# Kernel optimization log

Hardware: AMD Instinct MI355X
Metric: run time of the kernel (lower is better)

## Reference

```python
import jax, jax.numpy as jnp
import numpy as np

K = 5          # up_kernel
G = 1          # up_group
S = 2          # scale_factor


def conv2d(x, w, b, pad):
    y = jax.lax.conv_general_dilated(
        x, w, window_strides=(1, 1), padding=[(pad, pad), (pad, pad)],
        dimension_numbers=('NCHW', 'OIHW', 'NCHW'))
    return y + b[None, :, None, None]


def pixel_shuffle(x, r):
    n, c, h, w = x.shape
    x = x.reshape(n, c // (r * r), r, r, h, w)
    x = x.transpose(0, 1, 4, 2, 5, 3)  # n, c', h, r, w, r
    return x.reshape(n, c // (r * r), h * r, w * r)


def setup_inputs() -> dict:
    key = jax.random.key(0)
    k1, k2, k3 = jax.random.split(key, 3)
    x = jax.random.normal(k1, (8, 256, 64, 64), dtype=jnp.float32)
    w_comp = jax.random.normal(k2, (64, 256, 1, 1), dtype=jnp.float32) * 0.05
    b_comp = jnp.zeros((64,), dtype=jnp.float32)
    w_enc = jax.random.normal(k3, (100, 64, 3, 3), dtype=jnp.float32) * 0.001
    b_enc = jnp.zeros((100,), dtype=jnp.float32)
    return {"x": x, "w_comp": w_comp, "b_comp": b_comp, "w_enc": w_enc, "b_enc": b_enc}


def reference(x, w_comp, b_comp, w_enc, b_enc):
    n, c, h, w = x.shape
    kk = K * K
    # channel compressor (1x1) + content encoder (3x3, pad 1)
    comp = conv2d(x, w_comp, b_comp, pad=0)
    mask = conv2d(comp, w_enc, b_enc, pad=1)          # (n, kk*G*S*S, h, w)
    # kernel normalizer: pixel_shuffle then softmax over the kk taps
    mask = pixel_shuffle(mask, S)                      # (n, kk*G, H, W)
    H, W = h * S, w * S
    mask = mask.reshape(n, G, kk, H, W)
    mask = jax.nn.softmax(mask, axis=2)
    # CARAFE reassembly: each output pixel gathers KxK neighborhood of its
    # low-res source pixel (i//S, j//S) with the learned normalized weights.
    r = (K - 1) // 2
    xp = jnp.pad(x, ((0, 0), (0, 0), (r, r), (r, r)))
    cg = c // G
    out = jnp.zeros((n, c, H, W), dtype=x.dtype)
    for idx in range(kk):  # small fixed loop over kernel taps (25)
        dy, dx = idx // K, idx % K
        patch = xp[:, :, dy:dy + h, dx:dx + w]                     # (n,c,h,w)
        patch_up = jnp.repeat(jnp.repeat(patch, S, axis=2), S, axis=3)  # (n,c,H,W)
        wgt = mask[:, :, idx]                                      # (n,G,H,W)
        out = out + (patch_up.reshape(n, G, cg, H, W) * wgt[:, :, None]).reshape(n, c, H, W)
    return out
```

## Files before the change

kernel.cpp:

```cpp
#include <hip/hip_runtime.h>


#define CI 256

typedef __attribute__((ext_vector_type(8))) short bf16x8;
typedef __attribute__((ext_vector_type(4))) float f32x4;
typedef __attribute__((ext_vector_type(2))) float f32x2;

__device__ inline unsigned short f2bf(float f) {
    unsigned u = __float_as_uint(f);
    unsigned r = (u + 0x7FFF + ((u >> 16) & 1)) >> 16;
    return (unsigned short)r;
}

__device__ inline unsigned cvt_pk_bf16(float lo, float hi) {
    unsigned r;
    asm("v_cvt_pk_bf16_f32 %0, %1, %2" : "=v"(r) : "v"(lo), "v"(hi));
    return r;
}

__device__ inline float bf_lo(unsigned u) { return __int_as_float(u << 16); }
__device__ inline float bf_hi(unsigned u) { return __int_as_float(u & 0xffff0000u); }

__device__ inline void pk_fma_lo(f32x2& acc, f32x2 m, f32x2 s) {
    asm("v_pk_fma_f32 %0, %1, %2, %0 op_sel_hi:[1,0,1]" : "+v"(acc) : "v"(m), "v"(s));
}
__device__ inline void pk_fma_hi(f32x2& acc, f32x2 m, f32x2 s) {
    asm("v_pk_fma_f32 %0, %1, %2, %0 op_sel:[0,1,0] op_sel_hi:[1,1,1]" : "+v"(acc) : "v"(m), "v"(s));
}

__device__ inline void nt_store2(float* p, f32x2 v) {
    __builtin_nontemporal_store(__builtin_bit_cast(unsigned long long, v),
                                (unsigned long long*)p);
}

__global__ __launch_bounds__(256) void prep_small(const float* __restrict__ w_comp,
                                                  unsigned short* __restrict__ wA,
                                                  float* __restrict__ zp) {
    int i = blockIdx.x * 256 + threadIdx.x;
    if (i < 64) zp[i] = 0.f;
    if (i < 64 * 256) wA[i] = f2bf(w_comp[i]);
}

__global__ __launch_bounds__(64) void conv1x1_mfma(const float* __restrict__ x,
                                                   const unsigned short* __restrict__ wA,
                                                   const float* __restrict__ b_comp,
                                                   const float* __restrict__ w_enc,
                                                   unsigned short* __restrict__ comp,
                                                   unsigned short* __restrict__ Bp) {
    int l = threadIdx.x;
    int b = blockIdx.x;

    if (b >= 2048) {
        int idx = (b - 2048) * 64 + l;
        int j = idx & 7;
        int n = (idx >> 3) % 112;
        int g = idx / (112 * 8);
        int k = g * 8 + j;
        int tap = k >> 6;
        int c = k & 63;
        float v = (n < 100) ? w_enc[n * 576 + c * 9 + tap] : 0.f;
        Bp[idx] = f2bf(v);
        return;
    }

    int c16 = l & 15;
    int lq  = l >> 4;
    int bs  = (b & 7) * 256 + (b >> 3);
    int P0  = bs * 16;
    int nimg = P0 >> 12;
    int hw   = P0 & 4095;

    const float* xp = x + (size_t)nimg * CI * 4096 + hw + c16;

    f32x4 acc[4];
#pragma unroll
    for (int mt = 0; mt < 4; mt++) acc[mt] = f32x4{0.f, 0.f, 0.f, 0.f};

#pragma unroll
    for (int ks = 0; ks < 8; ks++) {
        int k0 = ks * 32 + lq * 8;
        float v[8];
#pragma unroll
        for (int j = 0; j < 8; j++) v[j] = xp[(size_t)(k0 + j) * 4096];
        bf16x8 xb;
#pragma unroll
        for (int j = 0; j < 8; j++) xb[j] = (short)f2bf(v[j]);
#pragma unroll
        for (int mt = 0; mt < 4; mt++) {
            bf16x8 wf = *(const bf16x8*)(wA + (mt * 16 + c16) * 256 + k0);
            acc[mt] = __builtin_amdgcn_mfma_f32_16x16x32_bf16(wf, xb, acc[mt], 0, 0, 0);
        }
    }

    unsigned short* cp = comp + (size_t)(P0 + c16) * 64;
#pragma unroll
    for (int mt = 0; mt < 4; mt++) {
        int och0 = mt * 16 + lq * 4;
        float4 bb = *reinterpret_cast<const float4*>(b_comp + och0);
        unsigned u0 = f2bf(acc[mt][0] + bb.x) | (f2bf(acc[mt][1] + bb.y) << 16);
        unsigned u1 = f2bf(acc[mt][2] + bb.z) | (f2bf(acc[mt][3] + bb.w) << 16);
        reinterpret_cast<uint2*>(cp + och0)[0] = uint2{u0, u1};
    }
}

__global__ __launch_bounds__(256) void conv3x3_mfma(const unsigned short* __restrict__ comp,
                                                    const unsigned short* __restrict__ Bp,
                                                    const float* __restrict__ b_enc,
                                                    const float* __restrict__ zp,
                                                    unsigned* __restrict__ maskP) {
    __shared__ char Bs[2][5 * 7168];
    int tid = threadIdx.x;
    int wv  = tid >> 6;
    int l   = tid & 63;
    int c16 = l & 15;
    int lq  = l >> 4;
    int b   = blockIdx.x;
    int bs  = (b & 7) * 64 + (b >> 3);
    int nimg = bs >> 6;
    int h    = bs & 63;
    int w0   = wv * 16;

    const char* cbase = (const char*)(comp + (size_t)nimg * 4096 * 64);
    const char* zpb   = (const char*)zp;
    const char* Bpb   = (const char*)Bp;

#define STAGEPH(s0_, cnt_, buf_)                                                          \
    {                                                                                     \
        const char* src_ = Bpb + (s0_)*7168 + l * 16;                                     \
        for (int inst_ = wv; inst_ < 7 * (cnt_); inst_ += 4) {                            \
            __builtin_amdgcn_global_load_lds(                                             \
                (const __attribute__((address_space(1))) void*)(src_ + inst_ * 1024),     \
                (__attribute__((address_space(3))) void*)(&Bs[buf_][inst_ * 1024]),       \
                16, 0, 0);                                                                \
        }                                                                                 \
    }

    f32x4 acc[7];
#pragma unroll
    for (int nt = 0; nt < 7; nt++) acc[nt] = f32x4{0.f, 0.f, 0.f, 0.f};

    const int dyt[9] = {-1, -1, -1, 0, 0, 0, 1, 1, 1};
    const int dxt[9] = {-1, 0, 1, -1, 0, 1, -1, 0, 1};

    STAGEPH(0, 5, 0);
    __syncthreads();

#pragma unroll
    for (int ph = 0; ph < 4; ph++) {
        int s0  = ph * 5;
        int cnt = (s0 + 5 <= 18) ? 5 : (18 - s0);
        int cur = ph & 1;
        if (ph < 3) {
            int ns0  = s0 + 5;
            int ncnt = (ns0 + 5 <= 18) ? 5 : (18 - ns0);
            STAGEPH(ns0, ncnt, cur ^ 1);
        }
        for (int ss = 0; ss < cnt; ss++) {
            int s = s0 + ss;
            int tap = s >> 1, half = s & 1;
            int hh = h + dyt[tap];
            int ww = w0 + c16 + dxt[tap];
            const char* ap = ((unsigned)hh < 64u && (unsigned)ww < 64u)
                                 ? cbase + (hh * 64 + ww) * 128 : zpb;
            bf16x8 a = *(const bf16x8*)(ap + lq * 16 + half * 64);

            bf16x8 bf[7];
#pragma unroll
            for (int nt = 0; nt < 7; nt++)
                bf[nt] = *(const bf16x8*)(&Bs[cur][ss * 7168 + (lq * 112 + nt * 16 + c16) * 16]);
#pragma unroll
            for (int nt = 0; nt < 7; nt++)
                acc[nt] = __builtin_amdgcn_mfma_f32_16x16x32_bf16(a, bf[nt], acc[nt], 0, 0, 0);
        }
        __syncthreads();
    }
#undef STAGEPH

    float bias[7];
#pragma unroll
    for (int nt = 0; nt < 7; nt++) {
        int n = nt * 16 + c16;
        bias[nt] = (n < 100) ? b_enc[n] : 0.f;
    }
    int nvalid = (c16 < 4) ? 7 : 6;

    unsigned* mbase = maskP + ((size_t)nimg * 64 + h) * 3200;

#pragma unroll
    for (int r = 0; r < 4; r++) {
        float v[7];
#pragma unroll
        for (int nt = 0; nt < 7; nt++) v[nt] = acc[nt][r] + bias[nt];
        float m = v[0];
#pragma unroll
        for (int nt = 1; nt < 7; nt++) if (nt < nvalid) m = fmaxf(m, v[nt]);
        m = fmaxf(m, __shfl_xor(m, 4));
        m = fmaxf(m, __shfl_xor(m, 8));
        float e[7];
        float s = 0.f;
#pragma unroll
        for (int nt = 0; nt < 7; nt++) {
            e[nt] = (nt < nvalid) ? __expf(v[nt] - m) : 0.f;
            s += e[nt];
        }
        s += __shfl_xor(s, 4);
        s += __shfl_xor(s, 8);
        float inv = 1.f / s;
        int wpix = w0 + lq * 4 + r;
#pragma unroll
        for (int nt = 0; nt < 7; nt++) {
            float mine = (nt < nvalid) ? e[nt] * inv : 0.f;
            float part = __shfl_xor(mine, 1);
            if (((c16 & 1) == 0) && (nt * 16 + c16) < 100) {
                unsigned pk = cvt_pk_bf16(mine, part);
                mbase[(nt * 8 + (c16 >> 1)) * 64 + wpix] = pk;
            }
        }
    }
}

__global__ __launch_bounds__(256) void reassemble(const float* __restrict__ x,
                                                  const unsigned* __restrict__ maskP,
                                                  float* __restrict__ out) {
    int lane = threadIdx.x & 63;
    int cq   = threadIdx.x >> 6;
    int b    = blockIdx.x;
    int bs   = (b & 7) * 256 + (b >> 3);
    int cgb  = bs & 3;
    int h    = (bs >> 2) & 63;
    int n    = bs >> 8;
    int c0   = cgb * 64 + cq * 16;

    const unsigned* mrow = maskP + ((size_t)n * 64 + h) * 3200 + lane;

    int   yy[5];
    float vmy[5], vmx[5];
#pragma unroll
    for (int d = 0; d < 5; d++) {
        int y  = h + d - 2;
        int xc = lane + d - 2;
        yy[d]  = min(max(y, 0), 63) * 64;
        vmy[d] = ((unsigned)y  < 64u) ? 1.f : 0.f;
        vmx[d] = ((unsigned)xc < 64u) ? 1.f : 0.f;
    }

    f32x2 msk2[50];
#pragma unroll
    for (int t = 0; t < 25; t++) {
        float f = vmy[t / 5] * vmx[t % 5];
        unsigned u0 = mrow[(2 * t + 0) * 64];
        unsigned u1 = mrow[(2 * t + 1) * 64];
        f32x2 m01, m23;
        m01.x = bf_lo(u0); m01.y = bf_hi(u0);
        m23.x = bf_lo(u1); m23.y = bf_hi(u1);
        msk2[2 * t + 0] = m01 * f;
        msk2[2 * t + 1] = m23 * f;
    }

    int idxm2 = ((lane - 2) & 63) << 2;
    int idxm1 = ((lane - 1) & 63) << 2;
    int idxp1 = ((lane + 1) & 63) << 2;
    int idxp2 = ((lane + 2) & 63) << 2;

    const float* xbase = x + ((size_t)(n * CI + c0)) * 4096 + lane;
    float*       obase = out + ((size_t)(n * CI + c0) * 128 + 2 * h) * 128 + 2 * lane;

    float ra[5], rb[5];
    unsigned pk[5];
#pragma unroll
    for (int d = 0; d < 5; d++) {
        ra[d] = xbase[yy[d]];
        rb[d] = xbase[4096 + yy[d]];
        pk[d] = cvt_pk_bf16(ra[d], rb[d]);
    }

    for (int p = 0; p < 8; p++) {
        const float* xn = xbase + (size_t)((p < 7) ? (2 * p + 2) : 0) * 4096;
        float na[5], nb[5];
#pragma unroll
        for (int d = 0; d < 5; d++) {
            na[d] = xn[yy[d]];
            nb[d] = xn[4096 + yy[d]];
        }

        f32x2 A0 = {0.f, 0.f}, A1 = {0.f, 0.f};
        f32x2 B0 = {0.f, 0.f}, B1 = {0.f, 0.f};
#pragma unroll
        for (int d = 0; d < 5; d++) {
            int pv = (int)pk[d];
            int sm2 = __builtin_amdgcn_ds_bpermute(idxm2, pv);
            int sm1 = __builtin_amdgcn_ds_bpermute(idxm1, pv);
            int sp1 = __builtin_amdgcn_ds_bpermute(idxp1, pv);
            int sp2 = __builtin_amdgcn_ds_bpermute(idxp2, pv);
            f32x2 s[5];
            s[0].x = bf_lo((unsigned)sm2); s[0].y = bf_hi((unsigned)sm2);
            s[1].x = bf_lo((unsigned)sm1); s[1].y = bf_hi((unsigned)sm1);
            s[2].x = ra[d];                s[2].y = rb[d];
            s[3].x = bf_lo((unsigned)sp1); s[3].y = bf_hi((unsigned)sp1);
            s[4].x = bf_lo((unsigned)sp2); s[4].y = bf_hi((unsigned)sp2);
            const f32x2* mk2 = msk2 + d * 10;
#pragma unroll
            for (int k = 0; k < 5; k++) {
                pk_fma_lo(A0, mk2[2 * k + 0], s[k]);
                pk_fma_lo(A1, mk2[2 * k + 1], s[k]);
                pk_fma_hi(B0, mk2[2 * k + 0], s[k]);
                pk_fma_hi(B1, mk2[2 * k + 1], s[k]);
            }
        }
        float* opa = obase + (size_t)(2 * p) * 16384;
        float* opb = opa + 16384;
        nt_store2(opa, A0);
        nt_store2(opa + 128, A1);
        nt_store2(opb, B0);
        nt_store2(opb + 128, B1);

#pragma unroll
        for (int d = 0; d < 5; d++) {
            ra[d] = na[d];
            rb[d] = nb[d];
            pk[d] = cvt_pk_bf16(na[d], nb[d]);
        }
    }
}

extern "C" void kernel_launch(void* const* d_in, const int* in_sizes, int n_in,
                              void* d_out, int out_size, void* d_ws, size_t ws_size,
                              hipStream_t stream) {
    const float* x      = (const float*)d_in[0];
    const float* w_comp = (const float*)d_in[1];
    const float* b_comp = (const float*)d_in[2];
    const float* w_enc  = (const float*)d_in[3];
    const float* b_enc  = (const float*)d_in[4];
    float* out = (float*)d_out;

    char* ws = (char*)d_ws;
    float*          zp    = (float*)(ws + 0);
    unsigned short* wA    = (unsigned short*)(ws + 256);
    unsigned short* Bp    = (unsigned short*)(ws + 33024);
    unsigned short* comp  = (unsigned short*)(ws + 162048);
    unsigned*       maskP = (unsigned*)(ws + 4356352);

    prep_small<<<64, 256, 0, stream>>>(w_comp, wA, zp);
    conv1x1_mfma<<<2048 + 1008, 64, 0, stream>>>(x, wA, b_comp, w_enc, comp, Bp);
    conv3x3_mfma<<<512, 256, 0, stream>>>(comp, Bp, b_enc, zp, maskP);
    reassemble<<<2048, 256, 0, stream>>>(x, maskP, out);
}
```

Measured before the change: 68.68 us.

## Split 1x1 conv K-reduction across two waves and shrink 3x3 weight staging phases

The 1x1 conv block now uses two waves that each reduce half of the 256 input channels, then combines the partial MFMA accumulators through shared memory before adding bias and storing. This doubles memory-level parallelism per block without launching more blocks. The 3x3 conv stages weights in six phases of three slices instead of four phases of five. That cuts LDS use per block, which may allow higher occupancy, at the cost of more barriers. The extra LDS round-trip and __syncthreads add some overhead to the 1x1 kernel.

```diff
diff --git a/kernel.cpp b/kernel.cpp
--- a/kernel.cpp
+++ b/kernel.cpp
@@ -42,17 +42,17 @@
     if (i < 64 * 256) wA[i] = f2bf(w_comp[i]);
 }
 
-__global__ __launch_bounds__(64) void conv1x1_mfma(const float* __restrict__ x,
-                                                   const unsigned short* __restrict__ wA,
-                                                   const float* __restrict__ b_comp,
-                                                   const float* __restrict__ w_enc,
-                                                   unsigned short* __restrict__ comp,
-                                                   unsigned short* __restrict__ Bp) {
-    int l = threadIdx.x;
-    int b = blockIdx.x;
+__global__ __launch_bounds__(128) void conv1x1_mfma(const float* __restrict__ x,
+                                                    const unsigned short* __restrict__ wA,
+                                                    const float* __restrict__ b_comp,
+                                                    const float* __restrict__ w_enc,
+                                                    unsigned short* __restrict__ comp,
+                                                    unsigned short* __restrict__ Bp) {
+    int tid = threadIdx.x;
+    int b   = blockIdx.x;
 
     if (b >= 2048) {
-        int idx = (b - 2048) * 64 + l;
+        int idx = (b - 2048) * 128 + tid;
         int j = idx & 7;
         int n = (idx >> 3) % 112;
         int g = idx / (112 * 8);
@@ -64,6 +64,9 @@
         return;
     }
 
+    __shared__ float red[4][64][4];
+    int wv  = tid >> 6;
+    int l   = tid & 63;
     int c16 = l & 15;
     int lq  = l >> 4;
     int bs  = (b & 7) * 256 + (b >> 3);
@@ -78,8 +81,8 @@
     for (int mt = 0; mt < 4; mt++) acc[mt] = f32x4{0.f, 0.f, 0.f, 0.f};
 
 #pragma unroll
-    for (int ks = 0; ks < 8; ks++) {
-        int k0 = ks * 32 + lq * 8;
+    for (int ks = 0; ks < 4; ks++) {
+        int k0 = (wv * 4 + ks) * 32 + lq * 8;
         float v[8];
 #pragma unroll
         for (int j = 0; j < 8; j++) v[j] = xp[(size_t)(k0 + j) * 4096];
@@ -93,14 +96,27 @@
         }
     }
 
-    unsigned short* cp = comp + (size_t)(P0 + c16) * 64;
-#pragma unroll
-    for (int mt = 0; mt < 4; mt++) {
-        int och0 = mt * 16 + lq * 4;
-        float4 bb = *reinterpret_cast<const float4*>(b_comp + och0);
-        unsigned u0 = f2bf(acc[mt][0] + bb.x) | (f2bf(acc[mt][1] + bb.y) << 16);
-        unsigned u1 = f2bf(acc[mt][2] + bb.z) | (f2bf(acc[mt][3] + bb.w) << 16);
-        reinterpret_cast<uint2*>(cp + och0)[0] = uint2{u0, u1};
+    if (wv == 1) {
+#pragma unroll
+        for (int mt = 0; mt < 4; mt++)
+            *reinterpret_cast<f32x4*>(&red[mt][l][0]) = acc[mt];
+    }
+    __syncthreads();
+    if (wv == 0) {
+        unsigned short* cp = comp + (size_t)(P0 + c16) * 64;
+#pragma unroll
+        for (int mt = 0; mt < 4; mt++) {
+            f32x4 part = *reinterpret_cast<const f32x4*>(&red[mt][l][0]);
+            int och0 = mt * 16 + lq * 4;
+            float4 bb = *reinterpret_cast<const float4*>(b_comp + och0);
+            float r0 = acc[mt][0] + part[0] + bb.x;
+            float r1 = acc[mt][1] + part[1] + bb.y;
+            float r2 = acc[mt][2] + part[2] + bb.z;
+            float r3 = acc[mt][3] + part[3] + bb.w;
+            unsigned u0 = f2bf(r0) | (f2bf(r1) << 16);
+            unsigned u1 = f2bf(r2) | (f2bf(r3) << 16);
+            reinterpret_cast<uint2*>(cp + och0)[0] = uint2{u0, u1};
+        }
     }
 }
 
@@ -109,7 +125,7 @@
                                                     const float* __restrict__ b_enc,
                                                     const float* __restrict__ zp,
                                                     unsigned* __restrict__ maskP) {
-    __shared__ char Bs[2][5 * 7168];
+    __shared__ char Bs[2][3 * 7168];
     int tid = threadIdx.x;
     int wv  = tid >> 6;
     int l   = tid & 63;
@@ -125,10 +141,10 @@
     const char* zpb   = (const char*)zp;
     const char* Bpb   = (const char*)Bp;
 
-#define STAGEPH(s0_, cnt_, buf_)                                                          \
+#define STAGEPH(s0_, buf_)                                                                \
     {                                                                                     \
         const char* src_ = Bpb + (s0_)*7168 + l * 16;                                     \
-        for (int inst_ = wv; inst_ < 7 * (cnt_); inst_ += 4) {                            \
+        for (int inst_ = wv; inst_ < 21; inst_ += 4) {                                    \
             __builtin_amdgcn_global_load_lds(                                             \
                 (const __attribute__((address_space(1))) void*)(src_ + inst_ * 1024),     \
                 (__attribute__((address_space(3))) void*)(&Bs[buf_][inst_ * 1024]),       \
@@ -143,20 +159,15 @@
     const int dyt[9] = {-1, -1, -1, 0, 0, 0, 1, 1, 1};
     const int dxt[9] = {-1, 0, 1, -1, 0, 1, -1, 0, 1};
 
-    STAGEPH(0, 5, 0);
+    STAGEPH(0, 0);
     __syncthreads();
 
 #pragma unroll
-    for (int ph = 0; ph < 4; ph++) {
-        int s0  = ph * 5;
-        int cnt = (s0 + 5 <= 18) ? 5 : (18 - s0);
+    for (int ph = 0; ph < 6; ph++) {
+        int s0  = ph * 3;
         int cur = ph & 1;
-        if (ph < 3) {
-            int ns0  = s0 + 5;
-            int ncnt = (ns0 + 5 <= 18) ? 5 : (18 - ns0);
-            STAGEPH(ns0, ncnt, cur ^ 1);
-        }
-        for (int ss = 0; ss < cnt; ss++) {
+        if (ph < 5) STAGEPH(s0 + 3, cur ^ 1);
+        for (int ss = 0; ss < 3; ss++) {
             int s = s0 + ss;
             int tap = s >> 1, half = s & 1;
             int hh = h + dyt[tap];
@@ -342,7 +353,7 @@
     unsigned*       maskP = (unsigned*)(ws + 4356352);
 
     prep_small<<<64, 256, 0, stream>>>(w_comp, wA, zp);
-    conv1x1_mfma<<<2048 + 1008, 64, 0, stream>>>(x, wA, b_comp, w_enc, comp, Bp);
+    conv1x1_mfma<<<2048 + 504, 128, 0, stream>>>(x, wA, b_comp, w_enc, comp, Bp);
     conv3x3_mfma<<<512, 256, 0, stream>>>(comp, Bp, b_enc, zp, maskP);
     reassemble<<<2048, 256, 0, stream>>>(x, maskP, out);
 }
```

New measurement: 69.68 us. About the same (+1.5%).

## Interchange reassembly loops to drop mask registers; shrink conv3x3 LDS staging phases

Applied to the files above, without the earlier changes.

The reassemble kernel now loops over the 5 kernel rows on the outside and the 8 channel pairs on the inside. It keeps 8x4 packed accumulators and only 10 mask values per row, instead of holding all 50 mask pairs plus a software-prefetched row of x in registers. The aim is lower VGPR pressure and higher occupancy, at the cost of losing the explicit prefetch of the next channel pair's loads. Separately, the conv3x3 weight staging uses 3-step phases (6 phases) instead of 5-step ones, which cuts the LDS footprint and adds more barriers.

```diff
diff --git a/kernel.cpp b/kernel.cpp
--- a/kernel.cpp
+++ b/kernel.cpp
@@ -109,7 +109,7 @@
                                                     const float* __restrict__ b_enc,
                                                     const float* __restrict__ zp,
                                                     unsigned* __restrict__ maskP) {
-    __shared__ char Bs[2][5 * 7168];
+    __shared__ char Bs[2][3 * 7168];
     int tid = threadIdx.x;
     int wv  = tid >> 6;
     int l   = tid & 63;
@@ -125,10 +125,10 @@
     const char* zpb   = (const char*)zp;
     const char* Bpb   = (const char*)Bp;
 
-#define STAGEPH(s0_, cnt_, buf_)                                                          \
+#define STAGEPH(s0_, buf_)                                                                \
     {                                                                                     \
         const char* src_ = Bpb + (s0_)*7168 + l * 16;                                     \
-        for (int inst_ = wv; inst_ < 7 * (cnt_); inst_ += 4) {                            \
+        for (int inst_ = wv; inst_ < 21; inst_ += 4) {                                    \
             __builtin_amdgcn_global_load_lds(                                             \
                 (const __attribute__((address_space(1))) void*)(src_ + inst_ * 1024),     \
                 (__attribute__((address_space(3))) void*)(&Bs[buf_][inst_ * 1024]),       \
@@ -143,20 +143,15 @@
     const int dyt[9] = {-1, -1, -1, 0, 0, 0, 1, 1, 1};
     const int dxt[9] = {-1, 0, 1, -1, 0, 1, -1, 0, 1};
 
-    STAGEPH(0, 5, 0);
+    STAGEPH(0, 0);
     __syncthreads();
 
 #pragma unroll
-    for (int ph = 0; ph < 4; ph++) {
-        int s0  = ph * 5;
-        int cnt = (s0 + 5 <= 18) ? 5 : (18 - s0);
+    for (int ph = 0; ph < 6; ph++) {
+        int s0  = ph * 3;
         int cur = ph & 1;
-        if (ph < 3) {
-            int ns0  = s0 + 5;
-            int ncnt = (ns0 + 5 <= 18) ? 5 : (18 - ns0);
-            STAGEPH(ns0, ncnt, cur ^ 1);
-        }
-        for (int ss = 0; ss < cnt; ss++) {
+        if (ph < 5) STAGEPH(s0 + 3, cur ^ 1);
+        for (int ss = 0; ss < 3; ss++) {
             int s = s0 + ss;
             int tap = s >> 1, half = s & 1;
             int hh = h + dyt[tap];
@@ -234,30 +229,6 @@
 
     const unsigned* mrow = maskP + ((size_t)n * 64 + h) * 3200 + lane;
 
-    int   yy[5];
-    float vmy[5], vmx[5];
-#pragma unroll
-    for (int d = 0; d < 5; d++) {
-        int y  = h + d - 2;
-        int xc = lane + d - 2;
-        yy[d]  = min(max(y, 0), 63) * 64;
-        vmy[d] = ((unsigned)y  < 64u) ? 1.f : 0.f;
-        vmx[d] = ((unsigned)xc < 64u) ? 1.f : 0.f;
-    }
-
-    f32x2 msk2[50];
-#pragma unroll
-    for (int t = 0; t < 25; t++) {
-        float f = vmy[t / 5] * vmx[t % 5];
-        unsigned u0 = mrow[(2 * t + 0) * 64];
-        unsigned u1 = mrow[(2 * t + 1) * 64];
-        f32x2 m01, m23;
-        m01.x = bf_lo(u0); m01.y = bf_hi(u0);
-        m23.x = bf_lo(u1); m23.y = bf_hi(u1);
-        msk2[2 * t + 0] = m01 * f;
-        msk2[2 * t + 1] = m23 * f;
-    }
-
     int idxm2 = ((lane - 2) & 63) << 2;
     int idxm1 = ((lane - 1) & 63) << 2;
     int idxp1 = ((lane + 1) & 63) << 2;
@@ -266,29 +237,45 @@
     const float* xbase = x + ((size_t)(n * CI + c0)) * 4096 + lane;
     float*       obase = out + ((size_t)(n * CI + c0) * 128 + 2 * h) * 128 + 2 * lane;
 
-    float ra[5], rb[5];
-    unsigned pk[5];
+    float vmx[5];
 #pragma unroll
     for (int d = 0; d < 5; d++) {
-        ra[d] = xbase[yy[d]];
-        rb[d] = xbase[4096 + yy[d]];
-        pk[d] = cvt_pk_bf16(ra[d], rb[d]);
-    }
-
-    for (int p = 0; p < 8; p++) {
-        const float* xn = xbase + (size_t)((p < 7) ? (2 * p + 2) : 0) * 4096;
-        float na[5], nb[5];
-#pragma unroll
-        for (int d = 0; d < 5; d++) {
-            na[d] = xn[yy[d]];
-            nb[d] = xn[4096 + yy[d]];
-        }
-
-        f32x2 A0 = {0.f, 0.f}, A1 = {0.f, 0.f};
-        f32x2 B0 = {0.f, 0.f}, B1 = {0.f, 0.f};
-#pragma unroll
-        for (int d = 0; d < 5; d++) {
-            int pv = (int)pk[d];
+        int xc = lane + d - 2;
+        vmx[d] = ((unsigned)xc < 64u) ? 1.f : 0.f;
+    }
+
+    f32x2 acc[8][4];
+#pragma unroll
+    for (int p = 0; p < 8; p++)
+#pragma unroll
+        for (int q = 0; q < 4; q++) acc[p][q] = f32x2{0.f, 0.f};
+
+#pragma unroll
+    for (int d = 0; d < 5; d++) {
+        int y   = h + d - 2;
+        int yo  = min(max(y, 0), 63) * 64;
+        float fy = ((unsigned)y < 64u) ? 1.f : 0.f;
+
+        f32x2 mskd[10];
+#pragma unroll
+        for (int k = 0; k < 5; k++) {
+            int t = d * 5 + k;
+            float f = fy * vmx[k];
+            unsigned u0 = mrow[(2 * t + 0) * 64];
+            unsigned u1 = mrow[(2 * t + 1) * 64];
+            f32x2 m01, m23;
+            m01.x = bf_lo(u0); m01.y = bf_hi(u0);
+            m23.x = bf_lo(u1); m23.y = bf_hi(u1);
+            mskd[2 * k + 0] = m01 * f;
+            mskd[2 * k + 1] = m23 * f;
+        }
+
+#pragma unroll
+        for (int p = 0; p < 8; p++) {
+            const float* xc = xbase + (size_t)(2 * p) * 4096;
+            float ra = xc[yo];
+            float rb = xc[4096 + yo];
+            int pv = (int)cvt_pk_bf16(ra, rb);
             int sm2 = __builtin_amdgcn_ds_bpermute(idxm2, pv);
             int sm1 = __builtin_amdgcn_ds_bpermute(idxm1, pv);
             int sp1 = __builtin_amdgcn_ds_bpermute(idxp1, pv);
@@ -296,31 +283,27 @@
             f32x2 s[5];
             s[0].x = bf_lo((unsigned)sm2); s[0].y = bf_hi((unsigned)sm2);
             s[1].x = bf_lo((unsigned)sm1); s[1].y = bf_hi((unsigned)sm1);
-            s[2].x = ra[d];                s[2].y = rb[d];
+            s[2].x = ra;                   s[2].y = rb;
             s[3].x = bf_lo((unsigned)sp1); s[3].y = bf_hi((unsigned)sp1);
             s[4].x = bf_lo((unsigned)sp2); s[4].y = bf_hi((unsigned)sp2);
-            const f32x2* mk2 = msk2 + d * 10;
 #pragma unroll
             for (int k = 0; k < 5; k++) {
-                pk_fma_lo(A0, mk2[2 * k + 0], s[k]);
-                pk_fma_lo(A1, mk2[2 * k + 1], s[k]);
-                pk_fma_hi(B0, mk2[2 * k + 0], s[k]);
-                pk_fma_hi(B1, mk2[2 * k + 1], s[k]);
+                pk_fma_lo(acc[p][0], mskd[2 * k + 0], s[k]);
+                pk_fma_lo(acc[p][1], mskd[2 * k + 1], s[k]);
+                pk_fma_hi(acc[p][2], mskd[2 * k + 0], s[k]);
+                pk_fma_hi(acc[p][3], mskd[2 * k + 1], s[k]);
             }
         }
+    }
+
+#pragma unroll
+    for (int p = 0; p < 8; p++) {
         float* opa = obase + (size_t)(2 * p) * 16384;
         float* opb = opa + 16384;
-        nt_store2(opa, A0);
-        nt_store2(opa + 128, A1);
-        nt_store2(opb, B0);
-        nt_store2(opb + 128, B1);
-
-#pragma unroll
-        for (int d = 0; d < 5; d++) {
-            ra[d] = na[d];
-            rb[d] = nb[d];
-            pk[d] = cvt_pk_bf16(na[d], nb[d]);
-        }
+        nt_store2(opa,       acc[p][0]);
+        nt_store2(opa + 128, acc[p][1]);
+        nt_store2(opb,       acc[p][2]);
+        nt_store2(opb + 128, acc[p][3]);
     }
 }
 
```

New measurement: 74.25 us. 1.08x slower.
